# Kernel tuning notes

Measured on AMD Instinct MI355X. Metric: run time of the kernel, lower is better.

Reference implementation:

```python
import jax, jax.numpy as jnp
import numpy as np

B, T, D = 4, 1024, 1024
H, HD = 16, 64
DFF = 4096
EPS = 1e-5


def _ln(x, g, b):
    mu = jnp.mean(x, axis=-1, keepdims=True)
    var = jnp.var(x, axis=-1, keepdims=True)
    return (x - mu) * jax.lax.rsqrt(var + EPS) * g + b


def _attn(q_in, kv_in, wq, bq, wk, bk, wv, bv, wo, bo):
    # q_in: [B,Tq,D], kv_in: [B,Tk,D]
    Tq, Tk = q_in.shape[1], kv_in.shape[1]
    q = (q_in @ wq + bq).reshape(B, Tq, H, HD).transpose(0, 2, 1, 3)
    k = (kv_in @ wk + bk).reshape(B, Tk, H, HD).transpose(0, 2, 1, 3)
    v = (kv_in @ wv + bv).reshape(B, Tk, H, HD).transpose(0, 2, 1, 3)
    att = jnp.einsum('bhqd,bhkd->bhqk', q, k) * (1.0 / np.sqrt(HD))
    causal = jnp.tril(jnp.ones((Tq, Tk), dtype=bool))
    att = jnp.where(causal, att, -jnp.inf)
    att = jax.nn.softmax(att, axis=-1)
    y = jnp.einsum('bhqk,bhkd->bhqd', att, v)
    y = y.transpose(0, 2, 1, 3).reshape(B, Tq, H * HD)
    return y @ wo + bo


def setup_inputs() -> dict:
    key = jax.random.key(0)
    ks = jax.random.split(key, 20)
    g = lambda k, shp, scale: (jax.random.normal(k, shp, jnp.float32) * scale)
    s_d = 1.0 / np.sqrt(D)
    s_f = 1.0 / np.sqrt(DFF)
    inp = {
        'x_encoder': jax.random.normal(ks[0], (B, T, D), jnp.float32),
        'x': jax.random.normal(ks[1], (B, T, D), jnp.float32),
        'ln1_g': jnp.ones((D,), jnp.float32), 'ln1_b': jnp.zeros((D,), jnp.float32),
        'ln2_g': jnp.ones((D,), jnp.float32), 'ln2_b': jnp.zeros((D,), jnp.float32),
        'sa_wq': g(ks[2], (D, D), s_d), 'sa_bq': jnp.zeros((D,), jnp.float32),
        'sa_wk': g(ks[3], (D, D), s_d), 'sa_bk': jnp.zeros((D,), jnp.float32),
        'sa_wv': g(ks[4], (D, D), s_d), 'sa_bv': jnp.zeros((D,), jnp.float32),
        'sa_wo': g(ks[5], (D, D), s_d), 'sa_bo': jnp.zeros((D,), jnp.float32),
        'ca_wq': g(ks[6], (D, D), s_d), 'ca_bq': jnp.zeros((D,), jnp.float32),
        'ca_wk': g(ks[7], (D, D), s_d), 'ca_bk': jnp.zeros((D,), jnp.float32),
        'ca_wv': g(ks[8], (D, D), s_d), 'ca_bv': jnp.zeros((D,), jnp.float32),
        'ca_wo': g(ks[9], (D, D), s_d), 'ca_bo': jnp.zeros((D,), jnp.float32),
        'mlp_w1': g(ks[10], (D, DFF), s_d), 'mlp_b1': jnp.zeros((DFF,), jnp.float32),
        'mlp_w2': g(ks[11], (DFF, D), s_f), 'mlp_b2': jnp.zeros((D,), jnp.float32),
    }
    return inp


def reference(x_encoder, x, ln1_g, ln1_b, ln2_g, ln2_b,
              sa_wq, sa_bq, sa_wk, sa_bk, sa_wv, sa_bv, sa_wo, sa_bo,
              ca_wq, ca_bq, ca_wk, ca_bk, ca_wv, ca_bv, ca_wo, ca_bo,
              mlp_w1, mlp_b1, mlp_w2, mlp_b2):
    # x = x + SelfAttn(ln1(x))
    x = x + _attn(_ln(x, ln1_g, ln1_b), _ln(x, ln1_g, ln1_b),
                  sa_wq, sa_bq, sa_wk, sa_bk, sa_wv, sa_bv, sa_wo, sa_bo)
    # x = x + CrossAttn(x_encoder, ln1(x))  (note: ln1 reused, causal mask on dec x enc)
    x = x + _attn(_ln(x, ln1_g, ln1_b), x_encoder,
                  ca_wq, ca_bq, ca_wk, ca_bk, ca_wv, ca_bv, ca_wo, ca_bo)
    # MLP with exact GELU (torch nn.GELU default)
    h = _ln(x, ln2_g, ln2_b)
    h = jax.nn.gelu(h @ mlp_w1 + mlp_b1, approximate=False) @ mlp_w2 + mlp_b2
    return x + h
```

## Files before the change

kernel.cpp:

```cpp
#include <hip/hip_runtime.h>
#include <hip/hip_bf16.h>

typedef __bf16 bf16;
typedef __attribute__((ext_vector_type(8))) __bf16 bf16x8;
typedef __attribute__((ext_vector_type(4))) float f32x4;

#define MFMA16(a, b, c) __builtin_amdgcn_mfma_f32_16x16x32_bf16(a, b, c, 0, 0, 0)

#define LGKM_FENCE()                                      \
  do {                                                    \
    asm volatile("s_waitcnt lgkmcnt(0)" ::: "memory");    \
    __builtin_amdgcn_sched_barrier(0);                    \
  } while (0)

#define SCHED0() __builtin_amdgcn_sched_barrier(0)
#define SBAR() __builtin_amdgcn_s_barrier()
#define PRIO(x) __builtin_amdgcn_s_setprio(x)

typedef __attribute__((address_space(1))) void gvoid;
typedef __attribute__((address_space(3))) void lvoid;
__device__ __forceinline__ void gl16(const bf16* g, bf16* l) {
  __builtin_amdgcn_global_load_lds((gvoid*)g, (lvoid*)l, 16, 0, 0);
}


struct WPtrs { const float* p[8]; };

__global__ __launch_bounds__(256) void wtrans8_k(WPtrs wp, bf16* __restrict__ dst) {
  const float* w = wp.p[blockIdx.z];
  bf16* wt = dst + (size_t)blockIdx.z * 1024 * 1024;
  __shared__ float t[32][33];
  const int tx = threadIdx.x & 31, ty = threadIdx.x >> 5;
  const int nb = blockIdx.x * 32, kb = blockIdx.y * 32;
  for (int i = 0; i < 4; ++i)
    t[ty + i * 8][tx] = w[(size_t)(kb + ty + i * 8) * 1024 + nb + tx];
  __syncthreads();
  for (int i = 0; i < 4; ++i)
    wt[(size_t)(nb + ty + i * 8) * 1024 + kb + tx] = (bf16)t[tx][ty + i * 8];
}

__global__ __launch_bounds__(256) void wtrans_k(const float* __restrict__ w,
                                                bf16* __restrict__ wt,
                                                int K, int N) {
  __shared__ float t[32][33];
  const int tx = threadIdx.x & 31, ty = threadIdx.x >> 5;
  const int nb = blockIdx.x * 32, kb = blockIdx.y * 32;
  for (int i = 0; i < 4; ++i)
    t[ty + i * 8][tx] = w[(size_t)(kb + ty + i * 8) * N + nb + tx];
  __syncthreads();
  for (int i = 0; i < 4; ++i)
    wt[(size_t)(nb + ty + i * 8) * K + kb + tx] = (bf16)t[tx][ty + i * 8];
}

__global__ __launch_bounds__(256) void tobf_k(const float* __restrict__ in,
                                              bf16* __restrict__ out) {
  const int i = blockIdx.x * 256 + threadIdx.x;
  const float4 v = ((const float4*)in)[i];
  bf16* o = out + (size_t)i * 4;
  o[0] = (bf16)v.x; o[1] = (bf16)v.y; o[2] = (bf16)v.z; o[3] = (bf16)v.w;
}

struct B5 { const float* s[5]; };
__global__ __launch_bounds__(256) void bpack_k(B5 bp, float* __restrict__ bq3,
                                               float* __restrict__ bkv2) {
  const int i = blockIdx.x;
  float* d = (i < 3) ? bq3 + i * 1024 : bkv2 + (i - 3) * 1024;
  ((float4*)d)[threadIdx.x] = ((const float4*)bp.s[i])[threadIdx.x];
}

__global__ __launch_bounds__(256) void ln_k(const float* __restrict__ x,
                                            const float* __restrict__ g,
                                            const float* __restrict__ bta,
                                            bf16* __restrict__ out) {
  const int row = blockIdx.x, tid = threadIdx.x;
  const float4 v = ((const float4*)(x + (size_t)row * 1024))[tid];
  float s = v.x + v.y + v.z + v.w;
  float sq = v.x * v.x + v.y * v.y + v.z * v.z + v.w * v.w;
  for (int d = 1; d < 64; d <<= 1) { s += __shfl_xor(s, d); sq += __shfl_xor(sq, d); }
  __shared__ float rs[4], rq[4];
  const int w = tid >> 6, lane = tid & 63;
  if (lane == 0) { rs[w] = s; rq[w] = sq; }
  __syncthreads();
  s = rs[0] + rs[1] + rs[2] + rs[3];
  sq = rq[0] + rq[1] + rq[2] + rq[3];
  const float mean = s * (1.0f / 1024.0f);
  const float var = sq * (1.0f / 1024.0f) - mean * mean;
  const float rstd = rsqrtf(var + 1e-5f);
  const float4 gv = ((const float4*)g)[tid];
  const float4 bv = ((const float4*)bta)[tid];
  bf16* o = out + (size_t)row * 1024 + tid * 4;
  o[0] = (bf16)((v.x - mean) * rstd * gv.x + bv.x);
  o[1] = (bf16)((v.y - mean) * rstd * gv.y + bv.y);
  o[2] = (bf16)((v.z - mean) * rstd * gv.z + bv.z);
  o[3] = (bf16)((v.w - mean) * rstd * gv.w + bv.w);
}

template <int EPI>
__global__ __launch_bounds__(256) void gemm_k(const bf16* __restrict__ A,
                                              const bf16* __restrict__ Bt,
                                              const float* __restrict__ bias,
                                              const float* __restrict__ res,
                                              void* __restrict__ o0,
                                              void* __restrict__ o1,
                                              void* __restrict__ o2,
                                              int K, int N) {
  __shared__ bf16 As[2][128 * 64];
  __shared__ bf16 Bs[2][128 * 64];
  const int tid = threadIdx.x;
  const int lane = tid & 63, w = tid >> 6;
  const int wr = w >> 1, wc = w & 1;
  const int l15 = lane & 15, l4 = lane >> 4;
  const int gx = gridDim.x;
  const int nwg = gx * gridDim.y;
  const int flat = blockIdx.x + blockIdx.y * gx;
  const int swz = (flat & 7) * (nwg >> 3) + (flat >> 3);
  const size_t bm = swz / gx, bn = swz % gx;
  const bf16* Ab = A + bm * 128 * (size_t)K;
  const bf16* Bb = Bt + bn * 128 * (size_t)K;

  const f32x4 zero4 = {0.f, 0.f, 0.f, 0.f};
  f32x4 acc[4][4];
  for (int m = 0; m < 4; ++m)
    for (int n = 0; n < 4; ++n) acc[m][n] = zero4;

  const int srow = lane >> 3;
  const int gck = ((lane & 7) ^ srow) * 8;
  auto stage = [&](int buf, int t) {
    const int kt = t * 64;
    for (int j = 0; j < 4; ++j) {
      const int row = w * 32 + j * 8 + srow;
      bf16* la = As[buf] + (w * 256 + j * 64 + lane) * 8;
      bf16* lb = Bs[buf] + (w * 256 + j * 64 + lane) * 8;
      gl16(Ab + (size_t)row * K + kt + gck, la);
      gl16(Bb + (size_t)row * K + kt + gck, lb);
    }
  };
  const int xr = l15 & 7;
  const int c0 = (l4 ^ xr) * 8, c1 = ((4 + l4) ^ xr) * 8;
  auto compute = [&](int buf) {
    bf16x8 af[4][2], bfr[4][2];
    for (int m = 0; m < 4; ++m) {
      const int ro = (wr * 64 + m * 16 + l15) * 64;
      af[m][0] = *(const bf16x8*)&As[buf][ro + c0];
      af[m][1] = *(const bf16x8*)&As[buf][ro + c1];
    }
    for (int n = 0; n < 4; ++n) {
      const int ro = (wc * 64 + n * 16 + l15) * 64;
      bfr[n][0] = *(const bf16x8*)&Bs[buf][ro + c0];
      bfr[n][1] = *(const bf16x8*)&Bs[buf][ro + c1];
    }
    PRIO(1);
    for (int m = 0; m < 4; ++m)
      for (int n = 0; n < 4; ++n) {
        acc[m][n] = MFMA16(af[m][0], bfr[n][0], acc[m][n]);
        acc[m][n] = MFMA16(af[m][1], bfr[n][1], acc[m][n]);
      }
    PRIO(0);
  };

  const int nt = K >> 6;
  stage(0, 0);
  stage(1, 1);
  int cur = 0;
  for (int t = 0; t < nt - 2; ++t) {
    asm volatile("s_waitcnt vmcnt(8)" ::: "memory");
    SBAR(); SCHED0();
    compute(cur);
    SCHED0(); SBAR(); SCHED0();
    stage(cur, t + 2);
    cur ^= 1;
  }
  asm volatile("s_waitcnt vmcnt(8)" ::: "memory");
  SBAR(); SCHED0();
  compute(cur);
  cur ^= 1;
  asm volatile("s_waitcnt vmcnt(0)" ::: "memory");
  SBAR(); SCHED0();
  compute(cur);

  for (int m = 0; m < 4; ++m) {
    const int row0 = (int)bm * 128 + wr * 64 + m * 16 + l4 * 4;
    for (int n = 0; n < 4; ++n) {
      const int col = (int)bn * 128 + wc * 64 + n * 16 + l15;
      const float bv = bias[col];
      for (int r = 0; r < 4; ++r) {
        const int row = row0 + r;
        const float v = acc[m][n][r] + bv;
        if constexpr (EPI == 0) {
          ((bf16*)o0)[(size_t)row * N + col] = (bf16)v;
        } else if constexpr (EPI == 2) {
          ((float*)o0)[(size_t)row * N + col] = v + res[(size_t)row * N + col];
        } else if constexpr (EPI == 3) {
          const float gl = 0.5f * v * (1.0f + erff(v * 0.70710678118f));
          ((bf16*)o0)[(size_t)row * N + col] = (bf16)gl;
        } else {
          const int which = col >> 10, c = col & 1023;
          const int nplain = (EPI == 4) ? 2 : 1;
          if (which < nplain) {
            bf16* op = (bf16*)(which == 0 ? o0 : o1);
            op[(size_t)row * 1024 + c] = (bf16)v;
          } else {
            bf16* op = (bf16*)((EPI == 4) ? o2 : o1);
            const int b = row >> 10, t = row & 1023;
            const int h = c >> 6, hd = c & 63;
            op[(size_t)((b * 16 + h) * 64 + hd) * 1024 + t] = (bf16)v;
          }
        }
      }
    }
  }
}

template <int EPI>
__global__ __launch_bounds__(256) void gemm64_k(const bf16* __restrict__ A,
                                                const bf16* __restrict__ Bt,
                                                const float* __restrict__ bias,
                                                const float* __restrict__ res,
                                                void* __restrict__ o0,
                                                int K, int N) {
  __shared__ bf16 As[2][128 * 64];
  __shared__ bf16 Bs[2][64 * 64];
  const int tid = threadIdx.x;
  const int lane = tid & 63, w = tid >> 6;
  const int l15 = lane & 15, l4 = lane >> 4;
  const int gx = gridDim.x;
  const int nwg = gx * gridDim.y;
  const int flat = blockIdx.x + blockIdx.y * gx;
  const int swz = (flat & 7) * (nwg >> 3) + (flat >> 3);
  const size_t bm = swz / gx, bn = swz % gx;
  const bf16* Ab = A + bm * 128 * (size_t)K;
  const bf16* Bb = Bt + bn * 64 * (size_t)K;

  const f32x4 zero4 = {0.f, 0.f, 0.f, 0.f};
  f32x4 acc[2][4];
  for (int m = 0; m < 2; ++m)
    for (int n = 0; n < 4; ++n) acc[m][n] = zero4;

  const int srow = lane >> 3;
  const int gck = ((lane & 7) ^ srow) * 8;
  auto stage = [&](int buf, int t) {
    const int kt = t * 64;
    for (int j = 0; j < 4; ++j) {
      const int row = w * 32 + j * 8 + srow;
      gl16(Ab + (size_t)row * K + kt + gck, As[buf] + (w * 256 + j * 64 + lane) * 8);
    }
    for (int j = 0; j < 2; ++j) {
      const int row = w * 16 + j * 8 + srow;
      gl16(Bb + (size_t)row * K + kt + gck, Bs[buf] + (w * 128 + j * 64 + lane) * 8);
    }
  };
  const int xr = l15 & 7;
  const int c0 = (l4 ^ xr) * 8, c1 = ((4 + l4) ^ xr) * 8;
  auto compute = [&](int buf) {
    bf16x8 af[2][2], bfr[4][2];
    for (int m = 0; m < 2; ++m) {
      const int ro = (w * 32 + m * 16 + l15) * 64;
      af[m][0] = *(const bf16x8*)&As[buf][ro + c0];
      af[m][1] = *(const bf16x8*)&As[buf][ro + c1];
    }
    for (int n = 0; n < 4; ++n) {
      const int ro = (n * 16 + l15) * 64;
      bfr[n][0] = *(const bf16x8*)&Bs[buf][ro + c0];
      bfr[n][1] = *(const bf16x8*)&Bs[buf][ro + c1];
    }
    PRIO(1);
    for (int m = 0; m < 2; ++m)
      for (int n = 0; n < 4; ++n) {
        acc[m][n] = MFMA16(af[m][0], bfr[n][0], acc[m][n]);
        acc[m][n] = MFMA16(af[m][1], bfr[n][1], acc[m][n]);
      }
    PRIO(0);
  };

  const int nt = K >> 6;
  stage(0, 0);
  stage(1, 1);
  int cur = 0;
  for (int t = 0; t < nt - 2; ++t) {
    asm volatile("s_waitcnt vmcnt(6)" ::: "memory");
    SBAR(); SCHED0();
    compute(cur);
    SCHED0(); SBAR(); SCHED0();
    stage(cur, t + 2);
    cur ^= 1;
  }
  asm volatile("s_waitcnt vmcnt(6)" ::: "memory");
  SBAR(); SCHED0();
  compute(cur);
  cur ^= 1;
  asm volatile("s_waitcnt vmcnt(0)" ::: "memory");
  SBAR(); SCHED0();
  compute(cur);

  for (int m = 0; m < 2; ++m) {
    const int row0 = (int)bm * 128 + w * 32 + m * 16 + l4 * 4;
    for (int n = 0; n < 4; ++n) {
      const int col = (int)bn * 64 + n * 16 + l15;
      const float bv = bias[col];
      for (int r = 0; r < 4; ++r) {
        const int row = row0 + r;
        const float v = acc[m][n][r] + bv;
        if constexpr (EPI == 0) {
          ((bf16*)o0)[(size_t)row * N + col] = (bf16)v;
        } else {
          ((float*)o0)[(size_t)row * N + col] = v + res[(size_t)row * N + col];
        }
      }
    }
  }
}

__global__ __launch_bounds__(512) void attn_k(const bf16* __restrict__ Q,
                                              const bf16* __restrict__ Kb,
                                              const bf16* __restrict__ Vt,
                                              bf16* __restrict__ O) {
  __shared__ bf16 Ks[2][64 * 64];
  __shared__ bf16 Vs[2][64 * 64];
  __shared__ bf16 Plds[8][16][72];
  const int bx = blockIdx.x, bh = blockIdx.y;
  const int b = bh >> 4, h = bh & 15;
  const int tid = threadIdx.x, lane = tid & 63, w = tid >> 6;
  const int myqt = (w < 4) ? bx : (15 - bx);
  const int qbase = myqt * 64 + (w & 3) * 16;
  const int l15 = lane & 15, l4 = lane >> 4;
  const int nt = 16 - bx;

  const bf16* Qp = Q + (size_t)(b * 1024 + qbase + l15) * 1024 + h * 64 + l4 * 8;
  bf16x8 qf0 = *(const bf16x8*)Qp;
  bf16x8 qf1 = *(const bf16x8*)(Qp + 32);
  for (int i = 0; i < 8; ++i) {
    qf0[i] = (bf16)((float)qf0[i] * 0.125f);
    qf1[i] = (bf16)((float)qf1[i] * 0.125f);
  }
  bf16x8 onesf;
  for (int i = 0; i < 8; ++i) onesf[i] = (bf16)1.0f;

  const f32x4 zero4 = {0.f, 0.f, 0.f, 0.f};
  f32x4 o[4], ol;
  float mrow[4];
  for (int d = 0; d < 4; ++d) o[d] = zero4;
  ol = zero4;
  for (int r = 0; r < 4; ++r) mrow[r] = -1e30f;

  const int qrow0 = qbase + l4 * 4;

  const int srow = tid >> 3;
  const int cg = (tid & 7) ^ (srow & 7);
  const bf16* Kg = Kb + (size_t)(b * 1024 + srow) * 1024 + h * 64 + cg * 8;
  const bf16* Vg = Vt + (size_t)(bh * 64 + srow) * 1024 + cg * 8;
  auto stage = [&](int buf, int t) {
    gl16(Kg + (size_t)t * 64 * 1024, Ks[buf] + tid * 8);
    gl16(Vg + t * 64, Vs[buf] + tid * 8);
  };

  const int xr = l15 & 7;
  const int fc0 = (l4 ^ xr) * 8, fc1 = ((4 + l4) ^ xr) * 8;

  auto compute = [&](int buf, int kt) {
    const int kbase = kt * 64;
    f32x4 s[4];
    for (int n = 0; n < 4; ++n) s[n] = zero4;
    PRIO(1);
    for (int n = 0; n < 4; ++n) {
      const int ro = (n * 16 + l15) * 64;
      const bf16x8 kf0 = *(const bf16x8*)&Ks[buf][ro + fc0];
      const bf16x8 kf1 = *(const bf16x8*)&Ks[buf][ro + fc1];
      s[n] = MFMA16(qf0, kf0, s[n]);
      s[n] = MFMA16(qf1, kf1, s[n]);
    }
    PRIO(0);
    if (kt == myqt) {
      for (int n = 0; n < 4; ++n) {
        const int kc = kbase + n * 16 + l15;
        for (int r = 0; r < 4; ++r)
          if (kc > qrow0 + r) s[n][r] = -1e30f;
      }
    }
    float mx[4];
    for (int r = 0; r < 4; ++r)
      mx[r] = fmaxf(fmaxf(s[0][r], s[1][r]), fmaxf(s[2][r], s[3][r]));
    for (int d0 = 1; d0 < 16; d0 <<= 1)
      for (int r = 0; r < 4; ++r) mx[r] = fmaxf(mx[r], __shfl_xor(mx[r], d0));
    float alpha[4];
    for (int r = 0; r < 4; ++r) {
      const float mnew = fmaxf(mrow[r], mx[r]);
      alpha[r] = __expf(mrow[r] - mnew);
      mrow[r] = mnew;
    }
    for (int n = 0; n < 4; ++n)
      for (int r = 0; r < 4; ++r) s[n][r] = __expf(s[n][r] - mrow[r]);
    for (int d = 0; d < 4; ++d)
      for (int r = 0; r < 4; ++r) o[d][r] *= alpha[r];
    for (int r = 0; r < 4; ++r) ol[r] *= alpha[r];

    LGKM_FENCE();
    for (int r = 0; r < 4; ++r)
      for (int n = 0; n < 4; ++n)
        Plds[w][l4 * 4 + r][n * 16 + l15] = (bf16)s[n][r];
    LGKM_FENCE();
    const bf16x8 pf0 = *(const bf16x8*)&Plds[w][l15][l4 * 8];
    const bf16x8 pf1 = *(const bf16x8*)&Plds[w][l15][32 + l4 * 8];

    PRIO(1);
    for (int d = 0; d < 4; ++d) {
      const int ro = (d * 16 + l15) * 64;
      const bf16x8 vf0 = *(const bf16x8*)&Vs[buf][ro + fc0];
      const bf16x8 vf1 = *(const bf16x8*)&Vs[buf][ro + fc1];
      o[d] = MFMA16(pf0, vf0, o[d]);
      o[d] = MFMA16(pf1, vf1, o[d]);
    }
    ol = MFMA16(pf0, onesf, ol);
    ol = MFMA16(pf1, onesf, ol);
    PRIO(0);
  };

  stage(0, 0);
  stage(1, 1);
  int cur = 0;
  for (int t = 0; t < nt - 2; ++t) {
    asm volatile("s_waitcnt vmcnt(2)" ::: "memory");
    SBAR(); SCHED0();
    if (t <= myqt) compute(cur, t);
    SCHED0(); SBAR(); SCHED0();
    stage(cur, t + 2);
    cur ^= 1;
  }
  asm volatile("s_waitcnt vmcnt(2)" ::: "memory");
  SBAR(); SCHED0();
  if (nt - 2 <= myqt) compute(cur, nt - 2);
  cur ^= 1;
  asm volatile("s_waitcnt vmcnt(0)" ::: "memory");
  SBAR(); SCHED0();
  if (nt - 1 <= myqt) compute(cur, nt - 1);

  for (int r = 0; r < 4; ++r) {
    const float inv = 1.0f / ol[r];
    for (int d = 0; d < 4; ++d) {
      O[(size_t)(b * 1024 + qbase + l4 * 4 + r) * 1024 + h * 64 + d * 16 + l15] =
          (bf16)(o[d][r] * inv);
    }
  }
}

extern "C" void kernel_launch(void* const* d_in, const int* in_sizes, int n_in,
                              void* d_out, int out_size, void* d_ws, size_t ws_size,
                              hipStream_t stream) {
  const float* x_enc = (const float*)d_in[0];
  const float* x     = (const float*)d_in[1];
  const float* ln1_g = (const float*)d_in[2];
  const float* ln1_b = (const float*)d_in[3];
  const float* ln2_g = (const float*)d_in[4];
  const float* ln2_b = (const float*)d_in[5];
  const float* sa_wq = (const float*)d_in[6];  const float* sa_bq = (const float*)d_in[7];
  const float* sa_wk = (const float*)d_in[8];  const float* sa_bk = (const float*)d_in[9];
  const float* sa_wv = (const float*)d_in[10]; const float* sa_bv = (const float*)d_in[11];
  const float* sa_wo = (const float*)d_in[12]; const float* sa_bo = (const float*)d_in[13];
  const float* ca_wq = (const float*)d_in[14]; const float* ca_bq = (const float*)d_in[15];
  const float* ca_wk = (const float*)d_in[16]; const float* ca_bk = (const float*)d_in[17];
  const float* ca_wv = (const float*)d_in[18]; const float* ca_bv = (const float*)d_in[19];
  const float* ca_wo = (const float*)d_in[20]; const float* ca_bo = (const float*)d_in[21];
  const float* mlp_w1 = (const float*)d_in[22]; const float* mlp_b1 = (const float*)d_in[23];
  const float* mlp_w2 = (const float*)d_in[24]; const float* mlp_b2 = (const float*)d_in[25];

  char* ws = (char*)d_ws;
  size_t off = 0;
  auto take = [&](size_t bytes) { char* p = ws + off; off += (bytes + 255) & ~(size_t)255; return p; };

  bf16* wt8 = (bf16*)take((size_t)8 * 1024 * 1024 * 2);
  bf16* w1t   = (bf16*)take((size_t)4096 * 1024 * 2);
  bf16* w2t   = (bf16*)take((size_t)1024 * 4096 * 2);
  bf16* lnbuf = (bf16*)take((size_t)4096 * 1024 * 2);
  bf16* xe_bf = (bf16*)take((size_t)4096 * 1024 * 2);
  bf16* Qb    = (bf16*)take((size_t)4096 * 1024 * 2);
  bf16* Kbf   = (bf16*)take((size_t)4096 * 1024 * 2);
  bf16* Vtb   = (bf16*)take((size_t)4096 * 1024 * 2);
  bf16* AOb   = (bf16*)take((size_t)4096 * 1024 * 2);
  float* x1   = (float*)take((size_t)4096 * 1024 * 4);
  float* x2   = (float*)take((size_t)4096 * 1024 * 4);
  bf16* Hb    = (bf16*)take((size_t)4096 * 4096 * 2);
  float* bq3  = (float*)take((size_t)3072 * 4);
  float* bkv2 = (float*)take((size_t)2048 * 4);

  bf16* wt[8];
  for (int i = 0; i < 8; ++i) wt[i] = wt8 + (size_t)i * 1024 * 1024;

  const dim3 blk(256);
  WPtrs wp = {{sa_wq, sa_wk, sa_wv, sa_wo, ca_wq, ca_wk, ca_wv, ca_wo}};
  wtrans8_k<<<dim3(32, 32, 8), blk, 0, stream>>>(wp, wt8);
  wtrans_k<<<dim3(128, 32), blk, 0, stream>>>(mlp_w1, w1t, 1024, 4096);
  wtrans_k<<<dim3(32, 128), blk, 0, stream>>>(mlp_w2, w2t, 4096, 1024);
  tobf_k<<<4096, blk, 0, stream>>>(x_enc, xe_bf);
  B5 bp = {{sa_bq, sa_bk, sa_bv, ca_bk, ca_bv}};
  bpack_k<<<5, blk, 0, stream>>>(bp, bq3, bkv2);

  ln_k<<<4096, blk, 0, stream>>>(x, ln1_g, ln1_b, lnbuf);
  gemm_k<4><<<dim3(24, 32), blk, 0, stream>>>(lnbuf, wt[0], bq3, nullptr,
                                              Qb, Kbf, Vtb, 1024, 3072);
  attn_k<<<dim3(8, 64), dim3(512), 0, stream>>>(Qb, Kbf, Vtb, AOb);
  gemm64_k<2><<<dim3(16, 32), blk, 0, stream>>>(AOb, wt[3], sa_bo, x, x1, 1024, 1024);

  ln_k<<<4096, blk, 0, stream>>>(x1, ln1_g, ln1_b, lnbuf);
  gemm64_k<0><<<dim3(16, 32), blk, 0, stream>>>(lnbuf, wt[4], ca_bq, nullptr, Qb, 1024, 1024);
  gemm_k<5><<<dim3(16, 32), blk, 0, stream>>>(xe_bf, wt[5], bkv2, nullptr,
                                              Kbf, Vtb, nullptr, 1024, 2048);
  attn_k<<<dim3(8, 64), dim3(512), 0, stream>>>(Qb, Kbf, Vtb, AOb);
  gemm64_k<2><<<dim3(16, 32), blk, 0, stream>>>(AOb, wt[7], ca_bo, x1, x2, 1024, 1024);

  ln_k<<<4096, blk, 0, stream>>>(x2, ln2_g, ln2_b, lnbuf);
  gemm_k<3><<<dim3(32, 32), blk, 0, stream>>>(lnbuf, w1t, mlp_b1, nullptr,
                                              Hb, nullptr, nullptr, 1024, 4096);
  gemm64_k<2><<<dim3(16, 32), blk, 0, stream>>>(Hb, w2t, mlp_b2, x2,
                                                (float*)d_out, 4096, 1024);

  (void)in_sizes; (void)n_in; (void)out_size; (void)ws_size;
}
```

Before: 358.8 us.

## Replace 128x128 GEMM with 256x256-tile 8-wave kernel with interleaved LDS staging

Replaces the 128x128 tile GEMM used for the fused QKV, cross-attention KV and MLP up-projection with a 256x256-tile kernel running 512 threads (8 waves). Each wave computes a 128x64 sub-tile in four quadrant phases, with LDS fragment reads and global-to-LDS staging interleaved between MFMA bursts under barriers. The aim is higher arithmetic intensity per loaded byte and better overlap of memory traffic with MFMA work. In exchange it uses 128KB of LDS and many more accumulator registers, and the large tiles produce small grids (128 to 256 blocks), which may underfill the GPU's compute units and hurt occupancy.

```diff
diff --git a/kernel.cpp b/kernel.cpp
--- a/kernel.cpp
+++ b/kernel.cpp
@@ -96,101 +96,128 @@
 }
 
 template <int EPI>
-__global__ __launch_bounds__(256) void gemm_k(const bf16* __restrict__ A,
-                                              const bf16* __restrict__ Bt,
-                                              const float* __restrict__ bias,
-                                              const float* __restrict__ res,
-                                              void* __restrict__ o0,
-                                              void* __restrict__ o1,
-                                              void* __restrict__ o2,
-                                              int K, int N) {
-  __shared__ bf16 As[2][128 * 64];
-  __shared__ bf16 Bs[2][128 * 64];
+__global__ __launch_bounds__(512, 2) void gemm256_k(const bf16* __restrict__ A,
+                                                    const bf16* __restrict__ Bt,
+                                                    const float* __restrict__ bias,
+                                                    void* __restrict__ o0,
+                                                    void* __restrict__ o1,
+                                                    void* __restrict__ o2,
+                                                    int K, int N) {
+  __shared__ bf16 As[2][2][128 * 64];
+  __shared__ bf16 Bs[2][2][128 * 64];
   const int tid = threadIdx.x;
   const int lane = tid & 63, w = tid >> 6;
-  const int wr = w >> 1, wc = w & 1;
+  const int wr = w >> 2, wc = w & 3;
   const int l15 = lane & 15, l4 = lane >> 4;
   const int gx = gridDim.x;
   const int nwg = gx * gridDim.y;
   const int flat = blockIdx.x + blockIdx.y * gx;
   const int swz = (flat & 7) * (nwg >> 3) + (flat >> 3);
   const size_t bm = swz / gx, bn = swz % gx;
-  const bf16* Ab = A + bm * 128 * (size_t)K;
-  const bf16* Bb = Bt + bn * 128 * (size_t)K;
+  const bf16* Ab = A + bm * 256 * (size_t)K;
+  const bf16* Bb = Bt + bn * 256 * (size_t)K;
 
   const f32x4 zero4 = {0.f, 0.f, 0.f, 0.f};
-  f32x4 acc[4][4];
-  for (int m = 0; m < 4; ++m)
+  f32x4 acc[8][4];
+  for (int m = 0; m < 8; ++m)
     for (int n = 0; n < 4; ++n) acc[m][n] = zero4;
 
-  const int srow = lane >> 3;
-  const int gck = ((lane & 7) ^ srow) * 8;
-  auto stage = [&](int buf, int t) {
-    const int kt = t * 64;
-    for (int j = 0; j < 4; ++j) {
-      const int row = w * 32 + j * 8 + srow;
-      bf16* la = As[buf] + (w * 256 + j * 64 + lane) * 8;
-      bf16* lb = Bs[buf] + (w * 256 + j * 64 + lane) * 8;
-      gl16(Ab + (size_t)row * K + kt + gck, la);
-      gl16(Bb + (size_t)row * K + kt + gck, lb);
-    }
-  };
+  const int srow = tid >> 3;
+  const int gck = ((tid & 7) ^ (srow & 7)) * 8;
+  auto stA = [&](int buf, int half, int t) {
+    const bf16* src = Ab + (size_t)(half * 128 + srow) * K + t * 64 + gck;
+    bf16* dst = &As[buf][half][tid * 8];
+    gl16(src, dst);
+    gl16(src + (size_t)64 * K, dst + 4096);
+  };
+  auto stB = [&](int buf, int half, int t) {
+    const bf16* src = Bb + (size_t)(half * 128 + srow) * K + t * 64 + gck;
+    bf16* dst = &Bs[buf][half][tid * 8];
+    gl16(src, dst);
+    gl16(src + (size_t)64 * K, dst + 4096);
+  };
+
   const int xr = l15 & 7;
-  const int c0 = (l4 ^ xr) * 8, c1 = ((4 + l4) ^ xr) * 8;
-  auto compute = [&](int buf) {
-    bf16x8 af[4][2], bfr[4][2];
-    for (int m = 0; m < 4; ++m) {
-      const int ro = (wr * 64 + m * 16 + l15) * 64;
-      af[m][0] = *(const bf16x8*)&As[buf][ro + c0];
-      af[m][1] = *(const bf16x8*)&As[buf][ro + c1];
-    }
+  const int ca0 = (l4 ^ xr) * 8, ca1 = ((4 + l4) ^ xr) * 8;
+  bf16x8 af[4][2];
+  bf16x8 bfr[2][2][2];
+  const int brow0 = (wc & 1) * 64;
+  auto ldA = [&](int buf, int mh) {
+#pragma unroll
+    for (int i = 0; i < 4; ++i) {
+      const int r = mh * 64 + i * 16 + l15;
+      af[i][0] = *(const bf16x8*)&As[buf][wr][r * 64 + ca0];
+      af[i][1] = *(const bf16x8*)&As[buf][wr][r * 64 + ca1];
+    }
+  };
+  auto ldB = [&](int buf, int nh) {
+#pragma unroll
+    for (int j = 0; j < 2; ++j) {
+      const int r = brow0 + (nh * 2 + j) * 16 + l15;
+      bfr[nh][j][0] = *(const bf16x8*)&Bs[buf][wc >> 1][r * 64 + ca0];
+      bfr[nh][j][1] = *(const bf16x8*)&Bs[buf][wc >> 1][r * 64 + ca1];
+    }
+  };
+  auto mfma16 = [&](int mh, int nh) {
+#pragma unroll
+    for (int i = 0; i < 4; ++i)
+#pragma unroll
+      for (int j = 0; j < 2; ++j) {
+        acc[mh * 4 + i][nh * 2 + j] =
+            MFMA16(af[i][0], bfr[nh][j][0], acc[mh * 4 + i][nh * 2 + j]);
+        acc[mh * 4 + i][nh * 2 + j] =
+            MFMA16(af[i][1], bfr[nh][j][1], acc[mh * 4 + i][nh * 2 + j]);
+      }
+  };
+
+  auto ktile = [&](int buf, int tstage, bool dostage) {
+    ldA(buf, 0); ldB(buf, 0); SCHED0();
+    SBAR();
+    LGKM_FENCE();
+    PRIO(1); mfma16(0, 0); PRIO(0); SCHED0();
+    SBAR();
+    ldB(buf, 1); SCHED0();
+    SBAR();
+    LGKM_FENCE();
+    PRIO(1); mfma16(0, 1); PRIO(0); SCHED0();
+    SBAR();
+    ldA(buf, 1);
+    if (dostage) { stB(buf, 0, tstage); stB(buf, 1, tstage); }
+    SCHED0();
+    SBAR();
+    LGKM_FENCE();
+    PRIO(1); mfma16(1, 0); PRIO(0); SCHED0();
+    SBAR();
+    if (dostage) { stA(buf, 0, tstage); stA(buf, 1, tstage); }
+    SCHED0();
+    SBAR();
+    PRIO(1); mfma16(1, 1); PRIO(0); SCHED0();
+    SBAR();
+  };
+
+  const int nt = K >> 6;
+  stA(0, 0, 0); stA(0, 1, 0); stB(0, 0, 0); stB(0, 1, 0);
+  stA(1, 0, 1); stA(1, 1, 1); stB(1, 0, 1); stB(1, 1, 1);
+  for (int t = 0; t < nt; ++t) {
+    const int buf = t & 1;
+    if (t < nt - 1) {
+      asm volatile("s_waitcnt vmcnt(8)" ::: "memory");
+    } else {
+      asm volatile("s_waitcnt vmcnt(0)" ::: "memory");
+    }
+    SBAR(); SCHED0();
+    ktile(buf, t + 2, t < nt - 2);
+  }
+
+  for (int m = 0; m < 8; ++m) {
+    const int row0 = (int)bm * 256 + wr * 128 + m * 16 + l4 * 4;
     for (int n = 0; n < 4; ++n) {
-      const int ro = (wc * 64 + n * 16 + l15) * 64;
-      bfr[n][0] = *(const bf16x8*)&Bs[buf][ro + c0];
-      bfr[n][1] = *(const bf16x8*)&Bs[buf][ro + c1];
-    }
-    PRIO(1);
-    for (int m = 0; m < 4; ++m)
-      for (int n = 0; n < 4; ++n) {
-        acc[m][n] = MFMA16(af[m][0], bfr[n][0], acc[m][n]);
-        acc[m][n] = MFMA16(af[m][1], bfr[n][1], acc[m][n]);
-      }
-    PRIO(0);
-  };
-
-  const int nt = K >> 6;
-  stage(0, 0);
-  stage(1, 1);
-  int cur = 0;
-  for (int t = 0; t < nt - 2; ++t) {
-    asm volatile("s_waitcnt vmcnt(8)" ::: "memory");
-    SBAR(); SCHED0();
-    compute(cur);
-    SCHED0(); SBAR(); SCHED0();
-    stage(cur, t + 2);
-    cur ^= 1;
-  }
-  asm volatile("s_waitcnt vmcnt(8)" ::: "memory");
-  SBAR(); SCHED0();
-  compute(cur);
-  cur ^= 1;
-  asm volatile("s_waitcnt vmcnt(0)" ::: "memory");
-  SBAR(); SCHED0();
-  compute(cur);
-
-  for (int m = 0; m < 4; ++m) {
-    const int row0 = (int)bm * 128 + wr * 64 + m * 16 + l4 * 4;
-    for (int n = 0; n < 4; ++n) {
-      const int col = (int)bn * 128 + wc * 64 + n * 16 + l15;
+      const int col = (int)bn * 256 + wc * 64 + n * 16 + l15;
       const float bv = bias[col];
       for (int r = 0; r < 4; ++r) {
         const int row = row0 + r;
         const float v = acc[m][n][r] + bv;
-        if constexpr (EPI == 0) {
-          ((bf16*)o0)[(size_t)row * N + col] = (bf16)v;
-        } else if constexpr (EPI == 2) {
-          ((float*)o0)[(size_t)row * N + col] = v + res[(size_t)row * N + col];
-        } else if constexpr (EPI == 3) {
+        if constexpr (EPI == 3) {
           const float gl = 0.5f * v * (1.0f + erff(v * 0.70710678118f));
           ((bf16*)o0)[(size_t)row * N + col] = (bf16)gl;
         } else {
@@ -494,21 +521,21 @@
   bpack_k<<<5, blk, 0, stream>>>(bp, bq3, bkv2);
 
   ln_k<<<4096, blk, 0, stream>>>(x, ln1_g, ln1_b, lnbuf);
-  gemm_k<4><<<dim3(24, 32), blk, 0, stream>>>(lnbuf, wt[0], bq3, nullptr,
-                                              Qb, Kbf, Vtb, 1024, 3072);
+  gemm256_k<4><<<dim3(12, 16), dim3(512), 0, stream>>>(lnbuf, wt[0], bq3,
+                                                       Qb, Kbf, Vtb, 1024, 3072);
   attn_k<<<dim3(8, 64), dim3(512), 0, stream>>>(Qb, Kbf, Vtb, AOb);
   gemm64_k<2><<<dim3(16, 32), blk, 0, stream>>>(AOb, wt[3], sa_bo, x, x1, 1024, 1024);
 
   ln_k<<<4096, blk, 0, stream>>>(x1, ln1_g, ln1_b, lnbuf);
   gemm64_k<0><<<dim3(16, 32), blk, 0, stream>>>(lnbuf, wt[4], ca_bq, nullptr, Qb, 1024, 1024);
-  gemm_k<5><<<dim3(16, 32), blk, 0, stream>>>(xe_bf, wt[5], bkv2, nullptr,
-                                              Kbf, Vtb, nullptr, 1024, 2048);
+  gemm256_k<5><<<dim3(8, 16), dim3(512), 0, stream>>>(xe_bf, wt[5], bkv2,
+                                                      Kbf, Vtb, nullptr, 1024, 2048);
   attn_k<<<dim3(8, 64), dim3(512), 0, stream>>>(Qb, Kbf, Vtb, AOb);
   gemm64_k<2><<<dim3(16, 32), blk, 0, stream>>>(AOb, wt[7], ca_bo, x1, x2, 1024, 1024);
 
   ln_k<<<4096, blk, 0, stream>>>(x2, ln2_g, ln2_b, lnbuf);
-  gemm_k<3><<<dim3(32, 32), blk, 0, stream>>>(lnbuf, w1t, mlp_b1, nullptr,
-                                              Hb, nullptr, nullptr, 1024, 4096);
+  gemm256_k<3><<<dim3(16, 16), dim3(512), 0, stream>>>(lnbuf, w1t, mlp_b1,
+                                                       Hb, nullptr, nullptr, 1024, 4096);
   gemm64_k<2><<<dim3(16, 32), blk, 0, stream>>>(Hb, w2t, mlp_b2, x2,
                                                 (float*)d_out, 4096, 1024);
 
```

New measurement: 427.9 us. 19.2% more time.
